# Optimization experiments

Hardware: AMD Instinct MI355X
Metric: run time of the kernel (lower is better)

Reference implementation:

```python
import jax, jax.numpy as jnp
import numpy as np

N_EMBD, N_HEAD, N_KV_HEAD = 1024, 16, 4
HEAD_DIM = N_EMBD // N_HEAD  # 64
VE_GATE_CH = 12
RMS_EPS = 1.1920929e-07  # torch fp32 finfo.eps (F.rms_norm default)


def setup_inputs() -> dict:
    key = jax.random.key(0)
    ks = jax.random.split(key, 8)
    B, S = 2, 2048
    x = jax.random.normal(ks[0], (B, S, N_EMBD), dtype=jnp.float32)
    ve = jax.random.normal(ks[1], (B, S, N_KV_HEAD * HEAD_DIM), dtype=jnp.float32)
    # RoPE cache
    half = HEAD_DIM // 2
    inv_freq = 1.0 / (10000.0 ** (np.arange(half, dtype=np.float32) / half))
    ang = np.arange(S, dtype=np.float32)[:, None] * inv_freq[None, :]  # [S, 32]
    cos = jnp.asarray(np.cos(ang))[:, None, :]  # [S,1,32]
    sin = jnp.asarray(np.sin(ang))[:, None, :]
    attention_mask = jnp.ones((B, S), dtype=jnp.int32)
    sc = 0.02
    Wq = sc * jax.random.normal(ks[2], (N_EMBD, N_EMBD), dtype=jnp.float32)
    Wk = sc * jax.random.normal(ks[3], (N_KV_HEAD * HEAD_DIM, N_EMBD), dtype=jnp.float32)
    Wv = sc * jax.random.normal(ks[4], (N_KV_HEAD * HEAD_DIM, N_EMBD), dtype=jnp.float32)
    Wproj = sc * jax.random.normal(ks[5], (N_EMBD, N_EMBD), dtype=jnp.float32)
    Wgate = sc * jax.random.normal(ks[6], (N_KV_HEAD, VE_GATE_CH), dtype=jnp.float32)
    return {"x": x, "ve": ve, "cos": cos, "sin": sin,
            "Wq": Wq, "Wk": Wk, "Wv": Wv, "Wproj": Wproj, "Wgate": Wgate,
            "attention_mask": attention_mask, "left_window": 1024}


def _rope(t, cos, sin):
    half = t.shape[-1] // 2
    t1, t2 = t[..., :half], t[..., half:]
    return jnp.concatenate([t1 * cos + t2 * sin, -t1 * sin + t2 * cos], axis=-1)


def _rms_norm(t):
    return t * jax.lax.rsqrt(jnp.mean(t * t, axis=-1, keepdims=True) + RMS_EPS)


def reference(x, ve, cos, sin, Wq, Wk, Wv, Wproj, Wgate, attention_mask, left_window):
    B, S, _ = x.shape
    q = (x @ Wq.T).reshape(B, S, N_HEAD, HEAD_DIM)
    k = (x @ Wk.T).reshape(B, S, N_KV_HEAD, HEAD_DIM)
    v = (x @ Wv.T).reshape(B, S, N_KV_HEAD, HEAD_DIM)
    # value-embedding gating: 3*sigmoid(linear(x[..., :12])) per kv head
    gate = 3.0 * jax.nn.sigmoid(x[..., :VE_GATE_CH] @ Wgate.T)  # [B,S,Hkv]
    v = v + gate[..., None] * ve.reshape(B, S, N_KV_HEAD, HEAD_DIM)
    q = _rms_norm(_rope(q, cos, sin)) * 1.2
    k = _rms_norm(_rope(k, cos, sin)) * 1.2
    q = q.transpose(0, 2, 1, 3)  # [B,H,S,hd]
    k = k.transpose(0, 2, 1, 3)  # [B,Hkv,S,hd]
    v = v.transpose(0, 2, 1, 3)
    rep = N_HEAD // N_KV_HEAD
    k = jnp.repeat(k, rep, axis=1)  # repeat_interleave over head dim
    v = jnp.repeat(v, rep, axis=1)
    # causal + sliding-window bias, materialized as in the original
    pos = jnp.arange(S)
    allowed = (pos[:, None] >= pos[None, :]) & ((pos[:, None] - pos[None, :]) < left_window)
    allowed = allowed[None, None] & attention_mask.astype(bool)[:, None, None, :]  # [B,1,S,S]
    neg = jnp.finfo(x.dtype).min
    bias = jnp.where(allowed, jnp.float32(0.0), neg).astype(x.dtype)
    scale = 1.0 / np.sqrt(HEAD_DIM)
    scores = jnp.einsum('bhqd,bhkd->bhqk', q, k) * scale + bias
    w = jax.nn.softmax(scores, axis=-1)
    y = jnp.einsum('bhqk,bhkd->bhqd', w, v)
    y = y.transpose(0, 2, 1, 3).reshape(B, S, N_EMBD)
    return y @ Wproj.T
```

## Files before the change

kernel.cpp:

```cpp
#include <hip/hip_runtime.h>
#include <hip/hip_bf16.h>

#define SS 2048
#define EE 1024
#define RMS_EPS 1.1920929e-07f

typedef short v8s __attribute__((ext_vector_type(8)));
typedef float v4f __attribute__((ext_vector_type(4)));

#define MFMA16 __builtin_amdgcn_mfma_f32_16x16x32_bf16

__device__ __forceinline__ ushort f2bf(float f){
    union { __hip_bfloat16 b; ushort u; } c; c.b = __float2bfloat16(f); return c.u;
}
__device__ __forceinline__ float bf2f(ushort u){
    union { uint u; float f; } c; c.u = ((uint)u) << 16; return c.f;
}
__device__ __forceinline__ void split8(const float* p, uint4& H, uint4& L){
    float4 a = *(const float4*)p, b = *(const float4*)(p+4);
    float v[8] = {a.x,a.y,a.z,a.w,b.x,b.y,b.z,b.w};
    ushort hs[8], ls[8];
#pragma unroll
    for (int e=0;e<8;e++){
        ushort h = f2bf(v[e]);
        hs[e] = h;
        ls[e] = f2bf(v[e] - bf2f(h));
    }
    H = *(uint4*)hs; L = *(uint4*)ls;
}

__global__ __launch_bounds__(256)
void qkv_kernel(const float* __restrict__ x, const float* __restrict__ ve,
                const float* __restrict__ Wq, const float* __restrict__ Wk,
                const float* __restrict__ Wv, const float* __restrict__ Wg,
                const float* __restrict__ cosb, const float* __restrict__ sinb,
                ushort* __restrict__ qhb, ushort* __restrict__ qlb,
                ushort* __restrict__ khb, ushort* __restrict__ klb,
                ushort* __restrict__ vhT, ushort* __restrict__ vlT)
{
    __shared__ ushort Axh[128*64];
    __shared__ ushort Axl[128*64];
    __shared__ ushort Bwh[64*64];
    __shared__ ushort Bwl[64*64];
    const int t = threadIdx.x;
    const int lane = t & 63, w = t >> 6;
    const int g = lane >> 4, ln = lane & 15;
    const int nt = blockIdx.x, mt = blockIdx.y;
    const float* W;
    if (nt < 16)      W = Wq + (size_t)nt*64*EE;
    else if (nt < 20) W = Wk + (size_t)(nt-16)*64*EE;
    else              W = Wv + (size_t)(nt-20)*64*EE;
    const v4f vzero = {0.f,0.f,0.f,0.f};
    v4f acc[2][4];
#pragma unroll
    for (int m=0;m<2;m++)
#pragma unroll
        for (int j=0;j<4;j++) acc[m][j] = vzero;

    const int sr = t>>3, sc = t&7;
    for (int kt = 0; kt < EE; kt += 64){
#pragma unroll
        for (int p2=0;p2<4;p2++){
            int rr = sr + 32*p2;
            uint4 H,L; split8(x + (size_t)(mt*128+rr)*EE + kt + sc*8, H, L);
            int off = rr*64 + ((sc ^ (rr&7))<<3);
            *(uint4*)&Axh[off] = H; *(uint4*)&Axl[off] = L;
        }
#pragma unroll
        for (int p2=0;p2<2;p2++){
            int rr = sr + 32*p2;
            uint4 H,L; split8(W + (size_t)rr*EE + kt + sc*8, H, L);
            int off = rr*64 + ((sc ^ (rr&7))<<3);
            *(uint4*)&Bwh[off] = H; *(uint4*)&Bwl[off] = L;
        }
        __syncthreads();
        v8s ah[2][2], al[2][2], bh[4][2], bl[4][2];
#pragma unroll
        for (int m=0;m<2;m++){
            int row = 32*w + 16*m + ln;
#pragma unroll
            for (int s=0;s<2;s++){
                int off = row*64 + (((4*s+g) ^ (row&7))<<3);
                ah[m][s] = *(v8s*)&Axh[off];
                al[m][s] = *(v8s*)&Axl[off];
            }
        }
#pragma unroll
        for (int j=0;j<4;j++){
            int row = 16*j + ln;
#pragma unroll
            for (int s=0;s<2;s++){
                int off = row*64 + (((4*s+g) ^ (row&7))<<3);
                bh[j][s] = *(v8s*)&Bwh[off];
                bl[j][s] = *(v8s*)&Bwl[off];
            }
        }
#pragma unroll
        for (int m=0;m<2;m++)
#pragma unroll
            for (int j=0;j<4;j++)
#pragma unroll
                for (int s=0;s<2;s++){
                    acc[m][j] = MFMA16(ah[m][s], bh[j][s], acc[m][j], 0,0,0);
                    acc[m][j] = MFMA16(ah[m][s], bl[j][s], acc[m][j], 0,0,0);
                    acc[m][j] = MFMA16(al[m][s], bh[j][s], acc[m][j], 0,0,0);
                }
        __syncthreads();
    }

#pragma unroll
    for (int m=0;m<2;m++){
#pragma unroll
        for (int r=0;r<4;r++){
            int srow = mt*128 + 32*w + 16*m + 4*g + r;
            int bb  = srow >> 11;
            int ss_ = srow & 2047;
            float v0 = acc[m][0][r], v1 = acc[m][1][r];
            float v2 = acc[m][2][r], v3 = acc[m][3][r];
            if (nt < 20){
                float c0 = cosb[ss_*32 + ln],      s0 = sinb[ss_*32 + ln];
                float c1 = cosb[ss_*32 + 16 + ln], s1 = sinb[ss_*32 + 16 + ln];
                float lo0 =  v0*c0 + v2*s0, hi0 = -v0*s0 + v2*c0;
                float lo1 =  v1*c1 + v3*s1, hi1 = -v1*s1 + v3*c1;
                float ssq = lo0*lo0 + hi0*hi0 + lo1*lo1 + hi1*hi1;
                ssq += __shfl_xor(ssq, 1); ssq += __shfl_xor(ssq, 2);
                ssq += __shfl_xor(ssq, 4); ssq += __shfl_xor(ssq, 8);
                float rs = rsqrtf(ssq*(1.f/64.f) + RMS_EPS) * 1.2f;
                size_t base = (nt < 16) ? ((size_t)(bb*16 + nt)*SS + ss_)*64
                                        : ((size_t)(bb*4 + (nt-16))*SS + ss_)*64;
                ushort* dh = (nt < 16) ? (qhb + base) : (khb + base);
                ushort* dl = (nt < 16) ? (qlb + base) : (klb + base);
                float o0 = lo0*rs, o1 = lo1*rs, o2 = hi0*rs, o3 = hi1*rs;
                ushort h0 = f2bf(o0), h1 = f2bf(o1), h2 = f2bf(o2), h3 = f2bf(o3);
                dh[ln]    = h0; dl[ln]    = f2bf(o0 - bf2f(h0));
                dh[16+ln] = h1; dl[16+ln] = f2bf(o1 - bf2f(h1));
                dh[32+ln] = h2; dl[32+ln] = f2bf(o2 - bf2f(h2));
                dh[48+ln] = h3; dl[48+ln] = f2bf(o3 - bf2f(h3));
            } else {
                int head = nt - 20;
                float gsum = 0.f;
                const float* xr = x + (size_t)srow * EE;
#pragma unroll
                for (int c = 0; c < 12; c++) gsum += xr[c] * Wg[head*12 + c];
                float gate = 3.f / (1.f + __expf(-gsum));
                const float* ver = ve + (size_t)srow*256 + head*64;
                size_t vbase = ((size_t)(bb*4 + head)*64)*SS + ss_;
                float dv[4] = {v0, v1, v2, v3};
#pragma unroll
                for (int j=0;j<4;j++){
                    int d = 16*j + ln;
                    float ov = dv[j] + gate*ver[d];
                    ushort hh = f2bf(ov);
                    vhT[vbase + (size_t)d*SS] = hh;
                    vlT[vbase + (size_t)d*SS] = f2bf(ov - bf2f(hh));
                }
            }
        }
    }
}

__global__ __launch_bounds__(256)
void attn_kernel(const ushort* __restrict__ qhb, const ushort* __restrict__ qlb,
                 const ushort* __restrict__ khb, const ushort* __restrict__ klb,
                 const ushort* __restrict__ vhT, const ushort* __restrict__ vlT,
                 const int* __restrict__ amask, const int* __restrict__ lwp,
                 ushort* __restrict__ yhb, ushort* __restrict__ ylb)
{
    __shared__ ushort SMEM[24576];
    __shared__ float mbias[64];
    ushort* Qh = SMEM;
    ushort* Ql = SMEM + 4096;
    ushort* Kh = SMEM + 8192;
    ushort* Kl = SMEM + 12288;
    ushort* Vh = SMEM + 16384;
    ushort* Vl = SMEM + 20480;
    const int t = threadIdx.x, lane = t & 63, w = t >> 6;
    const int g = lane >> 4, ln = lane & 15;
    const int qt = blockIdx.x, bh = blockIdx.y;
    const int b = bh >> 4, h = bh & 15, kvh = h >> 2;
    const int LW = lwp[0];
    const int q0 = qt*64;
    const ushort* Qhp = qhb + ((size_t)(b*16+h)*SS + q0)*64;
    const ushort* Qlp = qlb + ((size_t)(b*16+h)*SS + q0)*64;
    const ushort* Khp = khb + ((size_t)(b*4+kvh)*SS)*64;
    const ushort* Klp = klb + ((size_t)(b*4+kvh)*SS)*64;
    const ushort* Vhp = vhT + (size_t)(b*4+kvh)*64*SS;
    const ushort* Vlp = vlT + (size_t)(b*4+kvh)*64*SS;

    const int sr = t>>3, sc = t&7;
#pragma unroll
    for (int p2=0;p2<2;p2++){
        int rr = sr + 32*p2;
        int off = rr*64 + ((sc ^ (rr&7))<<3);
        *(uint4*)&Qh[off] = *(const uint4*)(Qhp + (size_t)rr*64 + sc*8);
        *(uint4*)&Ql[off] = *(const uint4*)(Qlp + (size_t)rr*64 + sc*8);
    }
    __syncthreads();
    v8s qfh[2], qfl[2];
    {
        int row = 16*w + ln;
#pragma unroll
        for (int s=0;s<2;s++){
            int off = row*64 + (((4*s+g) ^ (row&7))<<3);
            qfh[s] = *(v8s*)&Qh[off];
            qfl[s] = *(v8s*)&Ql[off];
        }
    }
    const int qg = q0 + 16*w + ln;
    const int keyk = (ln&3) ^ ((ln>>2)<<1);
    float m_r = -1e30f, l_r = 0.f;
    const v4f vzero = {0.f,0.f,0.f,0.f};
    v4f o[4];
#pragma unroll
    for (int dt=0;dt<4;dt++) o[dt] = vzero;

    int lo = q0 - LW + 1; if (lo < 0) lo = 0;
    for (int kt = lo>>6; kt <= qt; kt++){
        int k0 = kt*64;
        __syncthreads();
#pragma unroll
        for (int p2=0;p2<2;p2++){
            int rr = sr + 32*p2;
            int kkey = (rr&3) ^ (((rr>>3)&3)<<1);
            int koff = rr*64 + ((sc ^ kkey)<<3);
            *(uint4*)&Kh[koff] = *(const uint4*)(Khp + (size_t)(k0+rr)*64 + sc*8);
            *(uint4*)&Kl[koff] = *(const uint4*)(Klp + (size_t)(k0+rr)*64 + sc*8);
            int voff = rr*64 + ((sc ^ (rr&7))<<3);
            *(uint4*)&Vh[voff] = *(const uint4*)(Vhp + (size_t)rr*SS + k0 + sc*8);
            *(uint4*)&Vl[voff] = *(const uint4*)(Vlp + (size_t)rr*SS + k0 + sc*8);
        }
        if (t < 64) mbias[t] = amask[(b<<11) + k0 + t] ? 0.f : -3.0e38f;
        __syncthreads();

        float p[4][4];
#pragma unroll
        for (int tau=0;tau<4;tau++){
            v4f sa = vzero;
            int krow = 32*(tau&1) + 8*(ln>>2) + 4*(tau>>1) + (ln&3);
#pragma unroll
            for (int s=0;s<2;s++){
                int off = krow*64 + (((4*s+g) ^ keyk)<<3);
                v8s afh = *(v8s*)&Kh[off];
                v8s afl = *(v8s*)&Kl[off];
                sa = MFMA16(afh, qfh[s], sa, 0,0,0);
                sa = MFMA16(afh, qfl[s], sa, 0,0,0);
                sa = MFMA16(afl, qfh[s], sa, 0,0,0);
            }
#pragma unroll
            for (int r=0;r<4;r++) p[tau][r] = sa[r];
        }

        float pmax = -3.0e38f;
#pragma unroll
        for (int tau=0;tau<4;tau++)
#pragma unroll
            for (int r=0;r<4;r++){
                int kk  = 32*(tau&1) + 8*g + 4*(tau>>1) + r;
                int kgl = k0 + kk;
                float scv = p[tau][r]*0.125f + mbias[kk];
                bool ok = (kgl <= qg) && (qg - kgl < LW);
                scv = ok ? scv : -3.0e38f;
                p[tau][r] = scv;
                pmax = fmaxf(pmax, scv);
            }
        pmax = fmaxf(pmax, __shfl_xor(pmax,16));
        pmax = fmaxf(pmax, __shfl_xor(pmax,32));
        float mnew = fmaxf(m_r, pmax);
        float al = __expf(m_r - mnew);
        float ls = 0.f;
#pragma unroll
        for (int tau=0;tau<4;tau++)
#pragma unroll
            for (int r=0;r<4;r++){
                float e = __expf(p[tau][r] - mnew);
                p[tau][r] = e; ls += e;
            }
        ls += __shfl_xor(ls,16); ls += __shfl_xor(ls,32);
        m_r = mnew; l_r = l_r*al + ls;

        v8s pbh[2], pbl[2];
#pragma unroll
        for (int s=0;s<2;s++){
            v8s ph, pl;
#pragma unroll
            for (int e=0;e<8;e++){
                float val = p[2*(e>>2)+s][e&3];
                ushort hh = f2bf(val);
                ph[e] = (short)hh;
                pl[e] = (short)f2bf(val - bf2f(hh));
            }
            pbh[s]=ph; pbl[s]=pl;
        }
#pragma unroll
        for (int dt=0;dt<4;dt++){
            o[dt] = o[dt]*al;
            int drow = 16*dt + ln;
#pragma unroll
            for (int s=0;s<2;s++){
                int off = drow*64 + (((4*s+g) ^ (ln&7))<<3);
                v8s vfh = *(v8s*)&Vh[off];
                v8s vfl = *(v8s*)&Vl[off];
                o[dt] = MFMA16(vfh, pbh[s], o[dt], 0,0,0);
                o[dt] = MFMA16(vfh, pbl[s], o[dt], 0,0,0);
                o[dt] = MFMA16(vfl, pbh[s], o[dt], 0,0,0);
            }
        }
    }

    __syncthreads();
    float inv = (l_r > 0.f) ? (1.0f / l_r) : 0.f;
    float* Ot = (float*)SMEM;
#pragma unroll
    for (int dt=0;dt<4;dt++)
#pragma unroll
        for (int r=0;r<4;r++){
            int d = 16*dt + 4*g + r;
            Ot[d*68 + 16*w + ln] = o[dt][r]*inv;
        }
    __syncthreads();
    {
        int q = t>>2, dp = t&3;
        ushort th[16], tl[16];
#pragma unroll
        for (int i=0;i<16;i++){
            float val = Ot[(dp*16+i)*68 + q];
            ushort hh = f2bf(val);
            th[i] = hh;
            tl[i] = f2bf(val - bf2f(hh));
        }
        size_t doff = (size_t)(b*SS + q0 + q)*EE + h*64 + dp*16;
        *(uint4*)(yhb + doff)     = *(uint4*)&th[0];
        *(uint4*)(yhb + doff + 8) = *(uint4*)&th[8];
        *(uint4*)(ylb + doff)     = *(uint4*)&tl[0];
        *(uint4*)(ylb + doff + 8) = *(uint4*)&tl[8];
    }
}

__global__ __launch_bounds__(256)
void proj_kernel(const ushort* __restrict__ yhb, const ushort* __restrict__ ylb,
                 const float* __restrict__ Wp, float* __restrict__ out)
{
    __shared__ ushort Ayh[128*64];
    __shared__ ushort Ayl[128*64];
    __shared__ ushort Bh[64*64];
    __shared__ ushort Bl[64*64];
    const int t = threadIdx.x;
    const int lane = t & 63, w = t >> 6;
    const int g = lane >> 4, ln = lane & 15;
    const int nt = blockIdx.x, mt = blockIdx.y;
    const v4f vzero = {0.f,0.f,0.f,0.f};
    v4f acc[2][4];
#pragma unroll
    for (int m=0;m<2;m++)
#pragma unroll
        for (int j=0;j<4;j++) acc[m][j] = vzero;

    const int sr = t>>3, sc = t&7;
    for (int kt = 0; kt < EE; kt += 64){
#pragma unroll
        for (int p2=0;p2<4;p2++){
            int rr = sr + 32*p2;
            int off = rr*64 + ((sc ^ (rr&7))<<3);
            *(uint4*)&Ayh[off] = *(const uint4*)(yhb + (size_t)(mt*128+rr)*EE + kt + sc*8);
            *(uint4*)&Ayl[off] = *(const uint4*)(ylb + (size_t)(mt*128+rr)*EE + kt + sc*8);
        }
#pragma unroll
        for (int p2=0;p2<2;p2++){
            int rr = sr + 32*p2;
            uint4 H,L; split8(Wp + (size_t)(nt*64+rr)*EE + kt + sc*8, H, L);
            int off = rr*64 + ((sc ^ (rr&7))<<3);
            *(uint4*)&Bh[off] = H; *(uint4*)&Bl[off] = L;
        }
        __syncthreads();
        v8s ah[2][2], al[2][2], bh[4][2], bl[4][2];
#pragma unroll
        for (int m=0;m<2;m++){
            int row = 32*w + 16*m + ln;
#pragma unroll
            for (int s=0;s<2;s++){
                int off = row*64 + (((4*s+g) ^ (row&7))<<3);
                ah[m][s] = *(v8s*)&Ayh[off];
                al[m][s] = *(v8s*)&Ayl[off];
            }
        }
#pragma unroll
        for (int j=0;j<4;j++){
            int row = 16*j + ln;
#pragma unroll
            for (int s=0;s<2;s++){
                int off = row*64 + (((4*s+g) ^ (row&7))<<3);
                bh[j][s] = *(v8s*)&Bh[off];
                bl[j][s] = *(v8s*)&Bl[off];
            }
        }
#pragma unroll
        for (int m=0;m<2;m++)
#pragma unroll
            for (int j=0;j<4;j++)
#pragma unroll
                for (int s=0;s<2;s++){
                    acc[m][j] = MFMA16(ah[m][s], bh[j][s], acc[m][j], 0,0,0);
                    acc[m][j] = MFMA16(ah[m][s], bl[j][s], acc[m][j], 0,0,0);
                    acc[m][j] = MFMA16(al[m][s], bh[j][s], acc[m][j], 0,0,0);
                }
        __syncthreads();
    }

#pragma unroll
    for (int m=0;m<2;m++)
#pragma unroll
        for (int r=0;r<4;r++){
            size_t grow = (size_t)mt*128 + 32*w + 16*m + 4*g + r;
#pragma unroll
            for (int j=0;j<4;j++)
                out[grow*EE + nt*64 + 16*j + ln] = acc[m][j][r];
        }
}

extern "C" void kernel_launch(void* const* d_in, const int* in_sizes, int n_in,
                              void* d_out, int out_size, void* d_ws, size_t ws_size,
                              hipStream_t stream)
{
    (void)in_sizes; (void)n_in; (void)out_size; (void)ws_size;
    const float* x     = (const float*)d_in[0];
    const float* ve    = (const float*)d_in[1];
    const float* cosb  = (const float*)d_in[2];
    const float* sinb  = (const float*)d_in[3];
    const float* Wq    = (const float*)d_in[4];
    const float* Wk    = (const float*)d_in[5];
    const float* Wv    = (const float*)d_in[6];
    const float* Wp    = (const float*)d_in[7];
    const float* Wg    = (const float*)d_in[8];
    const int*   amask = (const int*)d_in[9];
    const int*   lw    = (const int*)d_in[10];

    char* ws = (char*)d_ws;
    ushort* qhb = (ushort*)(ws);
    ushort* qlb = (ushort*)(ws + ( 8u<<20));
    ushort* khb = (ushort*)(ws + (16u<<20));
    ushort* klb = (ushort*)(ws + (18u<<20));
    ushort* vhT = (ushort*)(ws + (20u<<20));
    ushort* vlT = (ushort*)(ws + (22u<<20));
    ushort* yhb = (ushort*)(ws + (24u<<20));
    ushort* ylb = (ushort*)(ws + (32u<<20));

    qkv_kernel<<<dim3(24,32), 256, 0, stream>>>(x, ve, Wq, Wk, Wv, Wg, cosb, sinb,
                                                qhb, qlb, khb, klb, vhT, vlT);
    attn_kernel<<<dim3(32,32), 256, 0, stream>>>(qhb, qlb, khb, klb, vhT, vlT,
                                                 amask, lw, yhb, ylb);
    proj_kernel<<<dim3(16,32), 256, 0, stream>>>(yhb, ylb, Wp, (float*)d_out);
}
```

Measured before the change: 296.0 us.

## Pre-split fp32 inputs and weights into bf16 hi/lo buffers before GEMMs

Adds a split_pre kernel that converts x, Wq/Wk/Wv and Wproj into bf16 hi/lo pairs once per call, so the QKV and projection GEMMs load pre-split bf16 tiles instead of redoing the split per tile in every block. The attention kernel also drops the Q staging through shared memory and loads Q fragments straight from global memory, which shrinks LDS use. The path is gated on workspace size and adds five extra launches plus extra global traffic for the split buffers.

```diff
diff --git a/kernel.cpp b/kernel.cpp
--- a/kernel.cpp
+++ b/kernel.cpp
@@ -30,9 +30,25 @@
 }
 
 __global__ __launch_bounds__(256)
+void split_pre(const float* __restrict__ s, ushort* __restrict__ dh,
+               ushort* __restrict__ dl, int n8)
+{
+    int i = blockIdx.x*256 + threadIdx.x;
+    if (i < n8){
+        uint4 H, L;
+        split8(s + (size_t)i*8, H, L);
+        *(uint4*)(dh + (size_t)i*8) = H;
+        *(uint4*)(dl + (size_t)i*8) = L;
+    }
+}
+
+template<bool PRE>
+__global__ __launch_bounds__(256)
 void qkv_kernel(const float* __restrict__ x, const float* __restrict__ ve,
                 const float* __restrict__ Wq, const float* __restrict__ Wk,
                 const float* __restrict__ Wv, const float* __restrict__ Wg,
+                const ushort* __restrict__ xh, const ushort* __restrict__ xl,
+                const ushort* __restrict__ Wch, const ushort* __restrict__ Wcl,
                 const float* __restrict__ cosb, const float* __restrict__ sinb,
                 ushort* __restrict__ qhb, ushort* __restrict__ qlb,
                 ushort* __restrict__ khb, ushort* __restrict__ klb,
@@ -62,16 +78,26 @@
 #pragma unroll
         for (int p2=0;p2<4;p2++){
             int rr = sr + 32*p2;
-            uint4 H,L; split8(x + (size_t)(mt*128+rr)*EE + kt + sc*8, H, L);
             int off = rr*64 + ((sc ^ (rr&7))<<3);
-            *(uint4*)&Axh[off] = H; *(uint4*)&Axl[off] = L;
+            if (PRE){
+                *(uint4*)&Axh[off] = *(const uint4*)(xh + (size_t)(mt*128+rr)*EE + kt + sc*8);
+                *(uint4*)&Axl[off] = *(const uint4*)(xl + (size_t)(mt*128+rr)*EE + kt + sc*8);
+            } else {
+                uint4 H,L; split8(x + (size_t)(mt*128+rr)*EE + kt + sc*8, H, L);
+                *(uint4*)&Axh[off] = H; *(uint4*)&Axl[off] = L;
+            }
         }
 #pragma unroll
         for (int p2=0;p2<2;p2++){
             int rr = sr + 32*p2;
-            uint4 H,L; split8(W + (size_t)rr*EE + kt + sc*8, H, L);
             int off = rr*64 + ((sc ^ (rr&7))<<3);
-            *(uint4*)&Bwh[off] = H; *(uint4*)&Bwl[off] = L;
+            if (PRE){
+                *(uint4*)&Bwh[off] = *(const uint4*)(Wch + (size_t)(nt*64+rr)*EE + kt + sc*8);
+                *(uint4*)&Bwl[off] = *(const uint4*)(Wcl + (size_t)(nt*64+rr)*EE + kt + sc*8);
+            } else {
+                uint4 H,L; split8(W + (size_t)rr*EE + kt + sc*8, H, L);
+                *(uint4*)&Bwh[off] = H; *(uint4*)&Bwl[off] = L;
+            }
         }
         __syncthreads();
         v8s ah[2][2], al[2][2], bh[4][2], bl[4][2];
@@ -166,14 +192,12 @@
                  const int* __restrict__ amask, const int* __restrict__ lwp,
                  ushort* __restrict__ yhb, ushort* __restrict__ ylb)
 {
-    __shared__ ushort SMEM[24576];
+    __shared__ ushort SMEM[16384];
     __shared__ float mbias[64];
-    ushort* Qh = SMEM;
-    ushort* Ql = SMEM + 4096;
-    ushort* Kh = SMEM + 8192;
-    ushort* Kl = SMEM + 12288;
-    ushort* Vh = SMEM + 16384;
-    ushort* Vl = SMEM + 20480;
+    ushort* Kh = SMEM;
+    ushort* Kl = SMEM + 4096;
+    ushort* Vh = SMEM + 8192;
+    ushort* Vl = SMEM + 12288;
     const int t = threadIdx.x, lane = t & 63, w = t >> 6;
     const int g = lane >> 4, ln = lane & 15;
     const int qt = blockIdx.x, bh = blockIdx.y;
@@ -187,23 +211,13 @@
     const ushort* Vhp = vhT + (size_t)(b*4+kvh)*64*SS;
     const ushort* Vlp = vlT + (size_t)(b*4+kvh)*64*SS;
 
-    const int sr = t>>3, sc = t&7;
-#pragma unroll
-    for (int p2=0;p2<2;p2++){
-        int rr = sr + 32*p2;
-        int off = rr*64 + ((sc ^ (rr&7))<<3);
-        *(uint4*)&Qh[off] = *(const uint4*)(Qhp + (size_t)rr*64 + sc*8);
-        *(uint4*)&Ql[off] = *(const uint4*)(Qlp + (size_t)rr*64 + sc*8);
-    }
-    __syncthreads();
     v8s qfh[2], qfl[2];
     {
         int row = 16*w + ln;
 #pragma unroll
         for (int s=0;s<2;s++){
-            int off = row*64 + (((4*s+g) ^ (row&7))<<3);
-            qfh[s] = *(v8s*)&Qh[off];
-            qfl[s] = *(v8s*)&Ql[off];
+            qfh[s] = *(const v8s*)(Qhp + (size_t)row*64 + (4*s+g)*8);
+            qfl[s] = *(const v8s*)(Qlp + (size_t)row*64 + (4*s+g)*8);
         }
     }
     const int qg = q0 + 16*w + ln;
@@ -214,6 +228,7 @@
 #pragma unroll
     for (int dt=0;dt<4;dt++) o[dt] = vzero;
 
+    const int sr = t>>3, sc = t&7;
     int lo = q0 - LW + 1; if (lo < 0) lo = 0;
     for (int kt = lo>>6; kt <= qt; kt++){
         int k0 = kt*64;
@@ -336,9 +351,11 @@
     }
 }
 
+template<bool PRE>
 __global__ __launch_bounds__(256)
 void proj_kernel(const ushort* __restrict__ yhb, const ushort* __restrict__ ylb,
-                 const float* __restrict__ Wp, float* __restrict__ out)
+                 const float* __restrict__ Wp, const ushort* __restrict__ Wph,
+                 const ushort* __restrict__ Wpl, float* __restrict__ out)
 {
     __shared__ ushort Ayh[128*64];
     __shared__ ushort Ayl[128*64];
@@ -367,9 +384,14 @@
 #pragma unroll
         for (int p2=0;p2<2;p2++){
             int rr = sr + 32*p2;
-            uint4 H,L; split8(Wp + (size_t)(nt*64+rr)*EE + kt + sc*8, H, L);
             int off = rr*64 + ((sc ^ (rr&7))<<3);
-            *(uint4*)&Bh[off] = H; *(uint4*)&Bl[off] = L;
+            if (PRE){
+                *(uint4*)&Bh[off] = *(const uint4*)(Wph + (size_t)(nt*64+rr)*EE + kt + sc*8);
+                *(uint4*)&Bl[off] = *(const uint4*)(Wpl + (size_t)(nt*64+rr)*EE + kt + sc*8);
+            } else {
+                uint4 H,L; split8(Wp + (size_t)(nt*64+rr)*EE + kt + sc*8, H, L);
+                *(uint4*)&Bh[off] = H; *(uint4*)&Bl[off] = L;
+            }
         }
         __syncthreads();
         v8s ah[2][2], al[2][2], bh[4][2], bl[4][2];
@@ -421,7 +443,7 @@
                               void* d_out, int out_size, void* d_ws, size_t ws_size,
                               hipStream_t stream)
 {
-    (void)in_sizes; (void)n_in; (void)out_size; (void)ws_size;
+    (void)in_sizes; (void)n_in; (void)out_size;
     const float* x     = (const float*)d_in[0];
     const float* ve    = (const float*)d_in[1];
     const float* cosb  = (const float*)d_in[2];
@@ -433,20 +455,51 @@
     const float* Wg    = (const float*)d_in[8];
     const int*   amask = (const int*)d_in[9];
     const int*   lw    = (const int*)d_in[10];
-
+    float* out = (float*)d_out;
     char* ws = (char*)d_ws;
-    ushort* qhb = (ushort*)(ws);
-    ushort* qlb = (ushort*)(ws + ( 8u<<20));
-    ushort* khb = (ushort*)(ws + (16u<<20));
-    ushort* klb = (ushort*)(ws + (18u<<20));
-    ushort* vhT = (ushort*)(ws + (20u<<20));
-    ushort* vlT = (ushort*)(ws + (22u<<20));
-    ushort* yhb = (ushort*)(ws + (24u<<20));
-    ushort* ylb = (ushort*)(ws + (32u<<20));
-
-    qkv_kernel<<<dim3(24,32), 256, 0, stream>>>(x, ve, Wq, Wk, Wv, Wg, cosb, sinb,
-                                                qhb, qlb, khb, klb, vhT, vlT);
-    attn_kernel<<<dim3(32,32), 256, 0, stream>>>(qhb, qlb, khb, klb, vhT, vlT,
-                                                 amask, lw, yhb, ylb);
-    proj_kernel<<<dim3(16,32), 256, 0, stream>>>(yhb, ylb, Wp, (float*)d_out);
-}
+
+    if (ws_size >= (size_t)(50u<<20)){
+        ushort* xh  = (ushort*)(ws);
+        ushort* xl  = (ushort*)(ws + ( 8u<<20));
+        ushort* Wch = (ushort*)(ws + (16u<<20));
+        ushort* Wcl = (ushort*)(ws + (19u<<20));
+        ushort* Wph = (ushort*)(ws + (22u<<20));
+        ushort* Wpl = (ushort*)(ws + (24u<<20));
+        ushort* qhb = (ushort*)(ws + (26u<<20));
+        ushort* qlb = (ushort*)(ws + (34u<<20));
+        ushort* khb = (ushort*)(ws + (42u<<20));
+        ushort* klb = (ushort*)(ws + (44u<<20));
+        ushort* vhT = (ushort*)(ws + (46u<<20));
+        ushort* vlT = (ushort*)(ws + (48u<<20));
+        ushort* yhb = xh;
+        ushort* ylb = xl;
+
+        split_pre<<<2048, 256, 0, stream>>>(x,  xh,  xl,  524288);
+        split_pre<<< 512, 256, 0, stream>>>(Wq, Wch, Wcl, 131072);
+        split_pre<<< 128, 256, 0, stream>>>(Wk, Wch + (size_t)1024*EE, Wcl + (size_t)1024*EE, 32768);
+        split_pre<<< 128, 256, 0, stream>>>(Wv, Wch + (size_t)1280*EE, Wcl + (size_t)1280*EE, 32768);
+        split_pre<<< 512, 256, 0, stream>>>(Wp, Wph, Wpl, 131072);
+
+        qkv_kernel<true><<<dim3(24,32), 256, 0, stream>>>(x, ve, Wq, Wk, Wv, Wg,
+                xh, xl, Wch, Wcl, cosb, sinb, qhb, qlb, khb, klb, vhT, vlT);
+        attn_kernel<<<dim3(32,32), 256, 0, stream>>>(qhb, qlb, khb, klb, vhT, vlT,
+                amask, lw, yhb, ylb);
+        proj_kernel<true><<<dim3(16,32), 256, 0, stream>>>(yhb, ylb, Wp, Wph, Wpl, out);
+    } else {
+        ushort* qhb = (ushort*)(ws);
+        ushort* qlb = (ushort*)(ws + ( 8u<<20));
+        ushort* khb = (ushort*)(ws + (16u<<20));
+        ushort* klb = (ushort*)(ws + (18u<<20));
+        ushort* vhT = (ushort*)(ws + (20u<<20));
+        ushort* vlT = (ushort*)(ws + (22u<<20));
+        ushort* yhb = (ushort*)(ws + (24u<<20));
+        ushort* ylb = (ushort*)(ws + (32u<<20));
+
+        qkv_kernel<false><<<dim3(24,32), 256, 0, stream>>>(x, ve, Wq, Wk, Wv, Wg,
+                nullptr, nullptr, nullptr, nullptr, cosb, sinb,
+                qhb, qlb, khb, klb, vhT, vlT);
+        attn_kernel<<<dim3(32,32), 256, 0, stream>>>(qhb, qlb, khb, klb, vhT, vlT,
+                amask, lw, yhb, ylb);
+        proj_kernel<false><<<dim3(16,32), 256, 0, stream>>>(yhb, ylb, Wp, nullptr, nullptr, out);
+    }
+}
```

Result: faster. 265.2 us (-10.4%).
